# Kernel tuning notes

Measured on AMD Instinct MI355X. Metric: run time of the kernel, lower is better.

## Reference

```python
import jax, jax.numpy as jnp
import numpy as np

N_NODES = 100000
N_EDGES = 640000
NUM_GRAPHS = 256
IN_DIM, HID_DIM, OUT_DIM = 128, 128, 64


def setup_inputs() -> dict:
    key = jax.random.key(0)
    ks = jax.random.split(key, 6)
    x = jax.random.normal(ks[0], (N_NODES, IN_DIM), dtype=jnp.float32)
    edge_index = jax.random.randint(ks[1], (2, N_EDGES), 0, N_NODES, dtype=jnp.int64)
    batch = jnp.sort(jax.random.randint(ks[2], (N_NODES,), 0, NUM_GRAPHS, dtype=jnp.int64))
    W1 = jax.random.normal(ks[3], (IN_DIM, HID_DIM), dtype=jnp.float32) * (1.0 / np.sqrt(IN_DIM))
    b1 = jnp.zeros((HID_DIM,), dtype=jnp.float32)
    W2 = jax.random.normal(ks[4], (HID_DIM, OUT_DIM), dtype=jnp.float32) * (1.0 / np.sqrt(HID_DIM))
    b2 = jnp.zeros((OUT_DIM,), dtype=jnp.float32)
    return {"x": x, "edge_index": edge_index, "batch": batch,
            "W1": W1, "b1": b1, "W2": W2, "b2": b2}


def gcn_conv(x, row, col, norm, W, b, n_nodes):
    # transform first (smaller of in/out handled by W), then gather-scale-scatter
    xw = x @ W                                   # [N, F_out]
    msgs = norm[:, None] * xw[row]               # [E+N, F_out]
    out = jax.ops.segment_sum(msgs, col, num_segments=n_nodes)
    return out + b


def reference(x, edge_index, batch, W1, b1, W2, b2):
    n = x.shape[0]
    # add self-loops (PyG GCNConv default)
    loops = jnp.arange(n, dtype=edge_index.dtype)
    row = jnp.concatenate([edge_index[0], loops])  # sources
    col = jnp.concatenate([edge_index[1], loops])  # targets
    # symmetric normalization D^-1/2 (A+I) D^-1/2
    deg = jax.ops.segment_sum(jnp.ones_like(col, dtype=x.dtype), col, num_segments=n)
    dinv = jnp.where(deg > 0, jax.lax.rsqrt(deg), 0.0)
    norm = dinv[row] * dinv[col]
    h = jax.nn.relu(gcn_conv(x, row, col, norm, W1, b1, n))
    h = gcn_conv(h, row, col, norm, W2, b2, n)
    # global mean pool over batch ids
    sums = jax.ops.segment_sum(h, batch, num_segments=NUM_GRAPHS)
    counts = jax.ops.segment_sum(jnp.ones((n,), dtype=h.dtype), batch, num_segments=NUM_GRAPHS)
    return sums / jnp.clip(counts, 1.0)[:, None]
```

## Files before the change

kernel.cpp:

```cpp
#include <hip/hip_runtime.h>
#include <hip/hip_bf16.h>


typedef __attribute__((ext_vector_type(8))) short short8;
typedef __attribute__((ext_vector_type(4))) float f32x4;

__device__ __forceinline__ void atomAddF(float* p, float v) { unsafeAtomicAdd(p, v); }

__device__ __forceinline__ unsigned short bf_rne(float f) {
  unsigned int u = __float_as_uint(f);
  return (unsigned short)((u + 0x7fffu + ((u >> 16) & 1u)) >> 16);
}
__device__ __forceinline__ float bf2f(unsigned short h) {
  return __uint_as_float(((unsigned int)h) << 16);
}

__global__ __launch_bounds__(256) void k_prepw(const float* __restrict__ W1,
    const float* __restrict__ W2,
    unsigned short* __restrict__ W1th, unsigned short* __restrict__ W1tl,
    unsigned short* __restrict__ W2th, unsigned short* __restrict__ W2tl) {
  int i = blockIdx.x * 256 + threadIdx.x;
  if (i < 16384) {
    int c = i >> 7, k = i & 127;
    float f = W1[k * 128 + c];
    unsigned short hi = bf_rne(f);
    W1th[i] = hi;
    W1tl[i] = bf_rne(f - bf2f(hi));
  } else if (i < 16384 + 8192) {
    int j = i - 16384;
    int c = j >> 7, k = j & 127;
    float f = W2[k * 64 + c];
    unsigned short hi = bf_rne(f);
    W2th[j] = hi;
    W2tl[j] = bf_rne(f - bf2f(hi));
  }
}

__global__ __launch_bounds__(256) void k_count(const int* __restrict__ col,
                                               int* __restrict__ deg, int E) {
  int e = blockIdx.x * 256 + threadIdx.x;
  if (e < E) atomicAdd(&deg[col[e]], 1);
}

__global__ __launch_bounds__(256) void k_blocksum(const int* __restrict__ deg,
                                                  int* __restrict__ partial, int N) {
  __shared__ int sh[256];
  int t = threadIdx.x, i = blockIdx.x * 256 + t;
  sh[t] = (i < N) ? deg[i] : 0;
  __syncthreads();
  for (int o = 128; o > 0; o >>= 1) {
    if (t < o) sh[t] += sh[t + o];
    __syncthreads();
  }
  if (t == 0) partial[blockIdx.x] = sh[0];
}

__global__ __launch_bounds__(512) void k_scanpartial(int* __restrict__ partial, int nb) {
  __shared__ int sh[512];
  int t = threadIdx.x;
  int v = (t < nb) ? partial[t] : 0;
  sh[t] = v;
  __syncthreads();
  for (int o = 1; o < 512; o <<= 1) {
    int x = (t >= o) ? sh[t - o] : 0;
    __syncthreads();
    sh[t] += x;
    __syncthreads();
  }
  if (t < nb) partial[t] = sh[t] - v;
}

__global__ __launch_bounds__(256) void k_scanblock(int* __restrict__ deg,
    const int* __restrict__ partial, int* __restrict__ off,
    float* __restrict__ dinv, int N) {
  __shared__ int sh[256];
  int t = threadIdx.x, b = blockIdx.x, i = b * 256 + t;
  int v = (i < N) ? deg[i] : 0;
  sh[t] = v;
  __syncthreads();
  for (int o = 1; o < 256; o <<= 1) {
    int x = (t >= o) ? sh[t - o] : 0;
    __syncthreads();
    sh[t] += x;
    __syncthreads();
  }
  if (i < N) {
    int excl = partial[b] + sh[t] - v;
    off[i] = excl;
    deg[i] = excl;
    dinv[i] = rsqrtf((float)v + 1.0f);
    if (i == N - 1) off[N] = excl + v;
  }
}

__global__ __launch_bounds__(256) void k_fillcsr(const int* __restrict__ rows,
    const int* __restrict__ cols, int* __restrict__ cursor,
    int* __restrict__ csrsrc, int E) {
  int e = blockIdx.x * 256 + threadIdx.x;
  if (e < E) {
    int pos = atomicAdd(&cursor[cols[e]], 1);
    csrsrc[pos] = rows[e];
  }
}

__global__ __launch_bounds__(256) void k_goff(const int* __restrict__ batch,
                                              int* __restrict__ goff, int N, int G) {
  int g = blockIdx.x * 256 + threadIdx.x;
  if (g > G) return;
  int lo = 0, hi = N;
  while (lo < hi) {
    int m = (lo + hi) >> 1;
    if (batch[m] < g) lo = m + 1; else hi = m;
  }
  goff[g] = lo;
}

__global__ __launch_bounds__(256) void k_gemm1_mfma(
    const float* __restrict__ x,
    const unsigned short* __restrict__ W1th, const unsigned short* __restrict__ W1tl,
    const float* __restrict__ dinv, float* __restrict__ y, int N)
{
  const int tid = threadIdx.x;
  const int w = tid >> 6, l = tid & 63;
  const int v0 = blockIdx.x * 64;
  const int l15 = l & 15, lh = l >> 4;

  short8 bh[2][4], bl[2][4];
#pragma unroll
  for (int ct = 0; ct < 2; ++ct) {
    int colr = 32 * w + 16 * ct + l15;
#pragma unroll
    for (int ks = 0; ks < 4; ++ks) {
      bh[ct][ks] = *(const short8*)(W1th + colr * 128 + ks * 32 + 8 * lh);
      bl[ct][ks] = *(const short8*)(W1tl + colr * 128 + ks * 32 + 8 * lh);
    }
  }

#pragma unroll
  for (int rt = 0; rt < 4; ++rt) {
    int arow = v0 + rt * 16 + l15; if (arow >= N) arow = N - 1;
    const float* ar = x + (size_t)arow * 128 + 8 * lh;
    f32x4 acc0 = {0.f, 0.f, 0.f, 0.f}, acc1 = {0.f, 0.f, 0.f, 0.f};
#pragma unroll
    for (int ks = 0; ks < 4; ++ks) {
      float4 fa = *(const float4*)(ar + ks * 32);
      float4 fb = *(const float4*)(ar + ks * 32 + 4);
      short8 ah, al;
      float v0f;
      v0f = fa.x; ah[0] = (short)bf_rne(v0f); al[0] = (short)bf_rne(v0f - bf2f((unsigned short)ah[0]));
      v0f = fa.y; ah[1] = (short)bf_rne(v0f); al[1] = (short)bf_rne(v0f - bf2f((unsigned short)ah[1]));
      v0f = fa.z; ah[2] = (short)bf_rne(v0f); al[2] = (short)bf_rne(v0f - bf2f((unsigned short)ah[2]));
      v0f = fa.w; ah[3] = (short)bf_rne(v0f); al[3] = (short)bf_rne(v0f - bf2f((unsigned short)ah[3]));
      v0f = fb.x; ah[4] = (short)bf_rne(v0f); al[4] = (short)bf_rne(v0f - bf2f((unsigned short)ah[4]));
      v0f = fb.y; ah[5] = (short)bf_rne(v0f); al[5] = (short)bf_rne(v0f - bf2f((unsigned short)ah[5]));
      v0f = fb.z; ah[6] = (short)bf_rne(v0f); al[6] = (short)bf_rne(v0f - bf2f((unsigned short)ah[6]));
      v0f = fb.w; ah[7] = (short)bf_rne(v0f); al[7] = (short)bf_rne(v0f - bf2f((unsigned short)ah[7]));
      acc0 = __builtin_amdgcn_mfma_f32_16x16x32_bf16(ah, bh[0][ks], acc0, 0, 0, 0);
      acc0 = __builtin_amdgcn_mfma_f32_16x16x32_bf16(al, bh[0][ks], acc0, 0, 0, 0);
      acc0 = __builtin_amdgcn_mfma_f32_16x16x32_bf16(ah, bl[0][ks], acc0, 0, 0, 0);
      acc1 = __builtin_amdgcn_mfma_f32_16x16x32_bf16(ah, bh[1][ks], acc1, 0, 0, 0);
      acc1 = __builtin_amdgcn_mfma_f32_16x16x32_bf16(al, bh[1][ks], acc1, 0, 0, 0);
      acc1 = __builtin_amdgcn_mfma_f32_16x16x32_bf16(ah, bl[1][ks], acc1, 0, 0, 0);
    }

    int r4 = v0 + rt * 16 + lh * 4;
    float4 d4 = *(const float4*)(dinv + r4);
    int col0 = 32 * w + l15;
#pragma unroll
    for (int reg = 0; reg < 4; ++reg) {
      int row = r4 + reg;
      if (row < N) {
        float dd = (reg == 0) ? d4.x : (reg == 1) ? d4.y : (reg == 2) ? d4.z : d4.w;
        y[(size_t)row * 128 + col0]      = acc0[reg] * dd;
        y[(size_t)row * 128 + col0 + 16] = acc1[reg] * dd;
      }
    }
  }
}

__global__ __launch_bounds__(256) void k_gemm2_fused_mfma(
    const float* __restrict__ y, const int* __restrict__ off,
    const int* __restrict__ src,
    const unsigned short* __restrict__ W2th, const unsigned short* __restrict__ W2tl,
    const float* __restrict__ dinv, const float* __restrict__ b1,
    float* __restrict__ z, int N)
{
  __shared__ unsigned short hh[64 * 128];
  __shared__ unsigned short hl[64 * 128];
  const int tid = threadIdx.x;
  const int w = tid >> 6, l = tid & 63;
  const int v0 = blockIdx.x * 64;
  const int l15 = l & 15, lh = l >> 4;

  short8 bh[4], bl[4];
  {
    int colr = 16 * w + l15;
#pragma unroll
    for (int ks = 0; ks < 4; ++ks) {
      bh[ks] = *(const short8*)(W2th + colr * 128 + ks * 32 + 8 * lh);
      bl[ks] = *(const short8*)(W2tl + colr * 128 + ks * 32 + 8 * lh);
    }
  }

  {
    int vn = tid >> 2;
    int c0 = (tid & 3) * 32;
    int vv = v0 + vn;
    int vc = (vv < N) ? vv : N - 1;
    float acc[32];
    {
      const float4* yr = (const float4*)(y + (size_t)vc * 128 + c0);
#pragma unroll
      for (int q = 0; q < 8; ++q) {
        float4 t = yr[q];
        acc[4*q+0] = t.x; acc[4*q+1] = t.y; acc[4*q+2] = t.z; acc[4*q+3] = t.w;
      }
    }
    int e0 = off[vc], e1 = off[vc + 1];
    int last = e1 - 1;
    for (int i = e0; i < e1; i += 2) {
      int i1 = i + 1;
      int u0 = src[i];
      int u1 = src[i1 <= last ? i1 : last];
      float m1 = (i1 <= last) ? 1.f : 0.f;
      const float4* p0 = (const float4*)(y + (size_t)u0 * 128 + c0);
      const float4* p1 = (const float4*)(y + (size_t)u1 * 128 + c0);
#pragma unroll
      for (int q = 0; q < 8; ++q) {
        float4 t0 = p0[q], t1 = p1[q];
        acc[4*q+0] += t0.x + m1 * t1.x;
        acc[4*q+1] += t0.y + m1 * t1.y;
        acc[4*q+2] += t0.z + m1 * t1.z;
        acc[4*q+3] += t0.w + m1 * t1.w;
      }
    }
    float d = dinv[vc];
#pragma unroll
    for (int s = 0; s < 4; ++s) {
      short8 oh, ol;
#pragma unroll
      for (int j = 0; j < 8; ++j) {
        int dim = c0 + s * 8 + j;
        float hv = fmaxf(fmaf(d, acc[s*8+j], b1[dim]), 0.f);
        unsigned short hb = bf_rne(hv);
        oh[j] = (short)hb;
        ol[j] = (short)bf_rne(hv - bf2f(hb));
      }
      int byte = (vn * 256 + (c0 + s * 8) * 2) ^ ((vn & 7) << 4);
      *(short8*)((char*)hh + byte) = oh;
      *(short8*)((char*)hl + byte) = ol;
    }
  }
  __syncthreads();

#pragma unroll
  for (int rt = 0; rt < 4; ++rt) {
    int row = rt * 16 + l15;
    const int swz = (row & 7) << 4;
    const int base = row * 256 + lh * 16;
    f32x4 acc = {0.f, 0.f, 0.f, 0.f};
#pragma unroll
    for (int ks = 0; ks < 4; ++ks) {
      int byte = (base + ks * 64) ^ swz;
      short8 ah = *(const short8*)((char*)hh + byte);
      short8 al = *(const short8*)((char*)hl + byte);
      acc = __builtin_amdgcn_mfma_f32_16x16x32_bf16(ah, bh[ks], acc, 0, 0, 0);
      acc = __builtin_amdgcn_mfma_f32_16x16x32_bf16(al, bh[ks], acc, 0, 0, 0);
      acc = __builtin_amdgcn_mfma_f32_16x16x32_bf16(ah, bl[ks], acc, 0, 0, 0);
    }

    int r4 = v0 + rt * 16 + lh * 4;
    float4 d4 = *(const float4*)(dinv + r4);
    int col = 16 * w + l15;
#pragma unroll
    for (int reg = 0; reg < 4; ++reg) {
      int rr = r4 + reg;
      if (rr < N) {
        float dd = (reg == 0) ? d4.x : (reg == 1) ? d4.y : (reg == 2) ? d4.z : d4.w;
        z[(size_t)rr * 64 + col] = acc[reg] * dd;
      }
    }
  }
}

__global__ __launch_bounds__(256) void k_aggpool(
    const float* __restrict__ z, const int* __restrict__ off,
    const int* __restrict__ src, const float* __restrict__ dinv,
    const int* __restrict__ goff, float* __restrict__ out, int N)
{
  int g = blockIdx.x >> 3, seg = blockIdx.x & 7;
  int w = threadIdx.x >> 6, lane = threadIdx.x & 63;
  int lo = goff[g], hi = goff[g + 1];
  float acc = 0.f;
  for (int v = lo + seg * 4 + w; v < hi; v += 32) {
    float sv = z[(size_t)v * 64 + lane];
    int e0 = off[v], e1 = off[v + 1];
    int last = e1 - 1;
    for (int i = e0; i < e1; i += 4) {
      int i1 = i + 1, i2 = i + 2, i3 = i + 3;
      int u0 = src[i];
      int u1 = src[i1 <= last ? i1 : last];
      int u2 = src[i2 <= last ? i2 : last];
      int u3 = src[i3 <= last ? i3 : last];
      float a0 = z[(size_t)u0 * 64 + lane];
      float a1 = z[(size_t)u1 * 64 + lane];
      float a2 = z[(size_t)u2 * 64 + lane];
      float a3 = z[(size_t)u3 * 64 + lane];
      sv += a0;
      sv += (i1 <= last) ? a1 : 0.f;
      sv += (i2 <= last) ? a2 : 0.f;
      sv += (i3 <= last) ? a3 : 0.f;
    }
    acc = fmaf(dinv[v], sv, acc);
  }
  atomAddF(out + (size_t)g * 64 + lane, acc);
}

__global__ __launch_bounds__(256) void k_final(float* __restrict__ out,
    const int* __restrict__ goff, const float* __restrict__ b2, int total) {
  int i = blockIdx.x * 256 + threadIdx.x;
  if (i >= total) return;
  int g = i >> 6, d = i & 63;
  int n = goff[g + 1] - goff[g];
  out[i] = (n > 0) ? out[i] / (float)n + b2[d] : 0.f;
}

extern "C" void kernel_launch(void* const* d_in, const int* in_sizes, int n_in,
                              void* d_out, int out_size, void* d_ws, size_t ws_size,
                              hipStream_t stream) {
  const float* x     = (const float*)d_in[0];
  const int*   eidx  = (const int*)d_in[1];
  const int*   batch = (const int*)d_in[2];
  const float* W1    = (const float*)d_in[3];
  const float* b1    = (const float*)d_in[4];
  const float* W2    = (const float*)d_in[5];
  const float* b2    = (const float*)d_in[6];
  float* out = (float*)d_out;

  const int N = in_sizes[2];
  const int E = in_sizes[1] / 2;
  const int G = out_size / 64;

  const int* rows = eidx;
  const int* cols = eidx + E;

  float* y   = (float*)d_ws;
  float* z   = y + (size_t)N * 128;
  unsigned short* W1th = (unsigned short*)(z + (size_t)N * 64);
  unsigned short* W1tl = W1th + 16384;
  unsigned short* W2th = W1tl + 16384;
  unsigned short* W2tl = W2th + 8192;
  float* dinv    = (float*)(W2tl + 8192);
  int*   deg     = (int*)(dinv + N);
  int*   off     = deg + N;
  int*   partial = off + N + 1;
  int*   goff    = partial + 512;
  int*   csrsrc  = goff + G + 1;

  const int B = 256;
  const int nb = (N + B - 1) / B;

  hipMemsetAsync(deg, 0, (size_t)N * sizeof(int), stream);
  hipMemsetAsync(d_out, 0, (size_t)out_size * sizeof(float), stream);

  k_prepw<<<(16384 + 8192 + B - 1) / B, B, 0, stream>>>(W1, W2, W1th, W1tl, W2th, W2tl);

  k_count<<<(E + B - 1) / B, B, 0, stream>>>(cols, deg, E);
  k_blocksum<<<nb, B, 0, stream>>>(deg, partial, N);
  k_scanpartial<<<1, 512, 0, stream>>>(partial, nb);
  k_scanblock<<<nb, B, 0, stream>>>(deg, partial, off, dinv, N);
  k_fillcsr<<<(E + B - 1) / B, B, 0, stream>>>(rows, cols, deg, csrsrc, E);
  k_goff<<<(G + 1 + B - 1) / B, B, 0, stream>>>(batch, goff, N, G);

  k_gemm1_mfma<<<(N + 63) / 64, B, 0, stream>>>(x, W1th, W1tl, dinv, y, N);
  k_gemm2_fused_mfma<<<(N + 63) / 64, B, 0, stream>>>(y, off, csrsrc, W2th, W2tl, dinv, b1, z, N);
  k_aggpool<<<G * 8, B, 0, stream>>>(z, off, csrsrc, dinv, goff, out, N);
  k_final<<<(out_size + B - 1) / B, B, 0, stream>>>(out, goff, b2, out_size);
}
```

Before: 355.3 us.

## Replace gather-based final aggregation with source-side scatter into per-block graph tables

Builds a second, source-sorted edge list that stores each edge's destination graph id and dinv packed into one word. The final layer then scatters each node's z row into per-block 256x64 shared-memory tables with LDS atomics, and a separate kernel reduces the tables, applies the mean and adds the bias. This removes the per-edge gather of z rows and the global atomics in pooling, at the cost of an extra count/scan/fill pass, a 64 MB block-table write and a truncated-mantissa dinv in the packed metadata. The gemm2 gather kernel also moves to 32-node tiles with 4-way edge unrolling and an occupancy hint.

```diff
diff --git a/kernel.cpp b/kernel.cpp
--- a/kernel.cpp
+++ b/kernel.cpp
@@ -4,8 +4,6 @@
 
 typedef __attribute__((ext_vector_type(8))) short short8;
 typedef __attribute__((ext_vector_type(4))) float f32x4;
-
-__device__ __forceinline__ void atomAddF(float* p, float v) { unsafeAtomicAdd(p, v); }
 
 __device__ __forceinline__ unsigned short bf_rne(float f) {
   unsigned int u = __float_as_uint(f);
@@ -36,10 +34,13 @@
   }
 }
 
-__global__ __launch_bounds__(256) void k_count(const int* __restrict__ col,
-                                               int* __restrict__ deg, int E) {
+__global__ __launch_bounds__(256) void k_count2(const int* __restrict__ rows,
+    const int* __restrict__ cols, int* __restrict__ deg, int* __restrict__ odeg, int E) {
   int e = blockIdx.x * 256 + threadIdx.x;
-  if (e < E) atomicAdd(&deg[col[e]], 1);
+  if (e < E) {
+    atomicAdd(&deg[cols[e]], 1);
+    atomicAdd(&odeg[rows[e]], 1);
+  }
 }
 
 __global__ __launch_bounds__(256) void k_blocksum(const int* __restrict__ deg,
@@ -88,7 +89,7 @@
     int excl = partial[b] + sh[t] - v;
     off[i] = excl;
     deg[i] = excl;
-    dinv[i] = rsqrtf((float)v + 1.0f);
+    if (dinv) dinv[i] = rsqrtf((float)v + 1.0f);
     if (i == N - 1) off[N] = excl + v;
   }
 }
@@ -100,6 +101,18 @@
   if (e < E) {
     int pos = atomicAdd(&cursor[cols[e]], 1);
     csrsrc[pos] = rows[e];
+  }
+}
+
+__global__ __launch_bounds__(256) void k_fillcsc(const int* __restrict__ rows,
+    const int* __restrict__ cols, int* __restrict__ ocursor,
+    const int* __restrict__ batch, const float* __restrict__ dinv,
+    unsigned int* __restrict__ meta, int E) {
+  int e = blockIdx.x * 256 + threadIdx.x;
+  if (e < E) {
+    int s = rows[e], d = cols[e];
+    int pos = atomicAdd(&ocursor[s], 1);
+    meta[pos] = ((unsigned int)batch[d] << 24) | (__float_as_uint(dinv[d]) >> 8);
   }
 }
 
@@ -178,65 +191,73 @@
   }
 }
 
-__global__ __launch_bounds__(256) void k_gemm2_fused_mfma(
+__global__ __launch_bounds__(256, 4) void k_gemm2_fused_mfma(
     const float* __restrict__ y, const int* __restrict__ off,
     const int* __restrict__ src,
     const unsigned short* __restrict__ W2th, const unsigned short* __restrict__ W2tl,
     const float* __restrict__ dinv, const float* __restrict__ b1,
     float* __restrict__ z, int N)
 {
-  __shared__ unsigned short hh[64 * 128];
-  __shared__ unsigned short hl[64 * 128];
+  __shared__ __align__(16) unsigned short hh[32 * 128];
+  __shared__ __align__(16) unsigned short hl[32 * 128];
   const int tid = threadIdx.x;
   const int w = tid >> 6, l = tid & 63;
-  const int v0 = blockIdx.x * 64;
+  const int v0 = blockIdx.x * 32;
   const int l15 = l & 15, lh = l >> 4;
 
-  short8 bh[4], bl[4];
   {
-    int colr = 16 * w + l15;
-#pragma unroll
-    for (int ks = 0; ks < 4; ++ks) {
-      bh[ks] = *(const short8*)(W2th + colr * 128 + ks * 32 + 8 * lh);
-      bl[ks] = *(const short8*)(W2tl + colr * 128 + ks * 32 + 8 * lh);
-    }
-  }
-
-  {
-    int vn = tid >> 2;
-    int c0 = (tid & 3) * 32;
+    int vn = tid >> 3;
+    int c0 = (tid & 7) << 4;
     int vv = v0 + vn;
     int vc = (vv < N) ? vv : N - 1;
-    float acc[32];
+    float acc[16];
     {
       const float4* yr = (const float4*)(y + (size_t)vc * 128 + c0);
 #pragma unroll
-      for (int q = 0; q < 8; ++q) {
+      for (int q = 0; q < 4; ++q) {
         float4 t = yr[q];
         acc[4*q+0] = t.x; acc[4*q+1] = t.y; acc[4*q+2] = t.z; acc[4*q+3] = t.w;
       }
     }
     int e0 = off[vc], e1 = off[vc + 1];
     int last = e1 - 1;
-    for (int i = e0; i < e1; i += 2) {
-      int i1 = i + 1;
+    for (int i = e0; i < e1; i += 4) {
+      int i1 = i + 1, i2 = i + 2, i3 = i + 3;
       int u0 = src[i];
       int u1 = src[i1 <= last ? i1 : last];
+      int u2 = src[i2 <= last ? i2 : last];
+      int u3 = src[i3 <= last ? i3 : last];
       float m1 = (i1 <= last) ? 1.f : 0.f;
+      float m2 = (i2 <= last) ? 1.f : 0.f;
+      float m3 = (i3 <= last) ? 1.f : 0.f;
       const float4* p0 = (const float4*)(y + (size_t)u0 * 128 + c0);
       const float4* p1 = (const float4*)(y + (size_t)u1 * 128 + c0);
-#pragma unroll
-      for (int q = 0; q < 8; ++q) {
-        float4 t0 = p0[q], t1 = p1[q];
-        acc[4*q+0] += t0.x + m1 * t1.x;
-        acc[4*q+1] += t0.y + m1 * t1.y;
-        acc[4*q+2] += t0.z + m1 * t1.z;
-        acc[4*q+3] += t0.w + m1 * t1.w;
-      }
+      const float4* p2 = (const float4*)(y + (size_t)u2 * 128 + c0);
+      const float4* p3 = (const float4*)(y + (size_t)u3 * 128 + c0);
+      float4 t00 = p0[0], t01 = p0[1], t02 = p0[2], t03 = p0[3];
+      float4 t10 = p1[0], t11 = p1[1], t12 = p1[2], t13 = p1[3];
+      float4 t20 = p2[0], t21 = p2[1], t22 = p2[2], t23 = p2[3];
+      float4 t30 = p3[0], t31 = p3[1], t32 = p3[2], t33 = p3[3];
+      acc[0]  += t00.x + m1*t10.x + m2*t20.x + m3*t30.x;
+      acc[1]  += t00.y + m1*t10.y + m2*t20.y + m3*t30.y;
+      acc[2]  += t00.z + m1*t10.z + m2*t20.z + m3*t30.z;
+      acc[3]  += t00.w + m1*t10.w + m2*t20.w + m3*t30.w;
+      acc[4]  += t01.x + m1*t11.x + m2*t21.x + m3*t31.x;
+      acc[5]  += t01.y + m1*t11.y + m2*t21.y + m3*t31.y;
+      acc[6]  += t01.z + m1*t11.z + m2*t21.z + m3*t31.z;
+      acc[7]  += t01.w + m1*t11.w + m2*t21.w + m3*t31.w;
+      acc[8]  += t02.x + m1*t12.x + m2*t22.x + m3*t32.x;
+      acc[9]  += t02.y + m1*t12.y + m2*t22.y + m3*t32.y;
+      acc[10] += t02.z + m1*t12.z + m2*t22.z + m3*t32.z;
+      acc[11] += t02.w + m1*t12.w + m2*t22.w + m3*t32.w;
+      acc[12] += t03.x + m1*t13.x + m2*t23.x + m3*t33.x;
+      acc[13] += t03.y + m1*t13.y + m2*t23.y + m3*t33.y;
+      acc[14] += t03.z + m1*t13.z + m2*t23.z + m3*t33.z;
+      acc[15] += t03.w + m1*t13.w + m2*t23.w + m3*t33.w;
     }
     float d = dinv[vc];
 #pragma unroll
-    for (int s = 0; s < 4; ++s) {
+    for (int s = 0; s < 2; ++s) {
       short8 oh, ol;
 #pragma unroll
       for (int j = 0; j < 8; ++j) {
@@ -251,10 +272,20 @@
       *(short8*)((char*)hl + byte) = ol;
     }
   }
-  __syncthreads();
-
-#pragma unroll
-  for (int rt = 0; rt < 4; ++rt) {
+
+  short8 bh[4], bl[4];
+  {
+    int colr = 16 * w + l15;
+#pragma unroll
+    for (int ks = 0; ks < 4; ++ks) {
+      bh[ks] = *(const short8*)(W2th + colr * 128 + ks * 32 + 8 * lh);
+      bl[ks] = *(const short8*)(W2tl + colr * 128 + ks * 32 + 8 * lh);
+    }
+  }
+  __syncthreads();
+
+#pragma unroll
+  for (int rt = 0; rt < 2; ++rt) {
     int row = rt * 16 + l15;
     const int swz = (row & 7) << 4;
     const int base = row * 256 + lh * 16;
@@ -283,46 +314,58 @@
   }
 }
 
-__global__ __launch_bounds__(256) void k_aggpool(
-    const float* __restrict__ z, const int* __restrict__ off,
-    const int* __restrict__ src, const float* __restrict__ dinv,
-    const int* __restrict__ goff, float* __restrict__ out, int N)
+#define NB_TAB 256
+__global__ __launch_bounds__(1024) void k_scatterpool(
+    const float* __restrict__ z, const int* __restrict__ ooff,
+    const unsigned int* __restrict__ meta, const int* __restrict__ batch,
+    const float* __restrict__ dinv, float* __restrict__ blocktab, int N)
 {
-  int g = blockIdx.x >> 3, seg = blockIdx.x & 7;
-  int w = threadIdx.x >> 6, lane = threadIdx.x & 63;
-  int lo = goff[g], hi = goff[g + 1];
-  float acc = 0.f;
-  for (int v = lo + seg * 4 + w; v < hi; v += 32) {
-    float sv = z[(size_t)v * 64 + lane];
-    int e0 = off[v], e1 = off[v + 1];
-    int last = e1 - 1;
-    for (int i = e0; i < e1; i += 4) {
-      int i1 = i + 1, i2 = i + 2, i3 = i + 3;
-      int u0 = src[i];
-      int u1 = src[i1 <= last ? i1 : last];
-      int u2 = src[i2 <= last ? i2 : last];
-      int u3 = src[i3 <= last ? i3 : last];
-      float a0 = z[(size_t)u0 * 64 + lane];
-      float a1 = z[(size_t)u1 * 64 + lane];
-      float a2 = z[(size_t)u2 * 64 + lane];
-      float a3 = z[(size_t)u3 * 64 + lane];
-      sv += a0;
-      sv += (i1 <= last) ? a1 : 0.f;
-      sv += (i2 <= last) ? a2 : 0.f;
-      sv += (i3 <= last) ? a3 : 0.f;
-    }
-    acc = fmaf(dinv[v], sv, acc);
-  }
-  atomAddF(out + (size_t)g * 64 + lane, acc);
-}
-
-__global__ __launch_bounds__(256) void k_final(float* __restrict__ out,
-    const int* __restrict__ goff, const float* __restrict__ b2, int total) {
+  __shared__ float tab[256 * 64];
+  for (int i = threadIdx.x; i < 16384; i += 1024) tab[i] = 0.f;
+  __syncthreads();
+
+  const int wid = threadIdx.x >> 6, lane = threadIdx.x & 63;
+  const int per = (N + NB_TAB - 1) / NB_TAB;
+  const int n0 = blockIdx.x * per;
+  const int n1 = (n0 + per < N) ? n0 + per : N;
+
+  for (int u = n0 + wid; u < n1; u += 16) {
+    float zd = z[(size_t)u * 64 + lane];
+    int e0 = ooff[u], e1 = ooff[u + 1];
+    for (int base = e0; base < e1; base += 64) {
+      int idx = base + lane;
+      unsigned int m = (idx < e1) ? meta[idx] : 0u;
+      int cnt = e1 - base; if (cnt > 64) cnt = 64;
+      for (int j = 0; j < cnt; ++j) {
+        unsigned int mj = (unsigned int)__shfl((int)m, j);
+        int gj = mj >> 24;
+        float cj = __uint_as_float(mj << 8);
+        atomicAdd(&tab[gj * 64 + lane], cj * zd);
+      }
+    }
+    atomicAdd(&tab[batch[u] * 64 + lane], dinv[u] * zd);
+  }
+  __syncthreads();
+  float* dst = blocktab + (size_t)blockIdx.x * 16384;
+  for (int i = threadIdx.x; i < 16384; i += 1024) dst[i] = tab[i];
+}
+
+__global__ __launch_bounds__(256) void k_redtab(const float* __restrict__ blocktab,
+    const int* __restrict__ goff, const float* __restrict__ b2,
+    float* __restrict__ out) {
   int i = blockIdx.x * 256 + threadIdx.x;
-  if (i >= total) return;
+  if (i >= 16384) return;
+  float s0 = 0.f, s1 = 0.f, s2 = 0.f, s3 = 0.f;
+  for (int b = 0; b < NB_TAB; b += 4) {
+    s0 += blocktab[(size_t)(b + 0) * 16384 + i];
+    s1 += blocktab[(size_t)(b + 1) * 16384 + i];
+    s2 += blocktab[(size_t)(b + 2) * 16384 + i];
+    s3 += blocktab[(size_t)(b + 3) * 16384 + i];
+  }
+  float s = (s0 + s1) + (s2 + s3);
   int g = i >> 6, d = i & 63;
   int n = goff[g + 1] - goff[g];
-  out[i] = (n > 0) ? out[i] / (float)n + b2[d] : 0.f;
+  out[i] = (n > 0) ? s / (float)n + b2[d] : 0.f;
 }
 
 extern "C" void kernel_launch(void* const* d_in, const int* in_sizes, int n_in,
@@ -352,28 +395,35 @@
   unsigned short* W2tl = W2th + 8192;
   float* dinv    = (float*)(W2tl + 8192);
   int*   deg     = (int*)(dinv + N);
-  int*   off     = deg + N;
-  int*   partial = off + N + 1;
+  int*   odeg    = deg + N;
+  int*   off     = odeg + N;
+  int*   ooff    = off + N + 1;
+  int*   partial = ooff + N + 1;
   int*   goff    = partial + 512;
   int*   csrsrc  = goff + G + 1;
+  unsigned int* cscmeta = (unsigned int*)(csrsrc + E);
+  float* blocktab = (float*)(cscmeta + E);
 
   const int B = 256;
   const int nb = (N + B - 1) / B;
 
-  hipMemsetAsync(deg, 0, (size_t)N * sizeof(int), stream);
-  hipMemsetAsync(d_out, 0, (size_t)out_size * sizeof(float), stream);
+  hipMemsetAsync(deg, 0, (size_t)2 * N * sizeof(int), stream);
 
   k_prepw<<<(16384 + 8192 + B - 1) / B, B, 0, stream>>>(W1, W2, W1th, W1tl, W2th, W2tl);
 
-  k_count<<<(E + B - 1) / B, B, 0, stream>>>(cols, deg, E);
+  k_count2<<<(E + B - 1) / B, B, 0, stream>>>(rows, cols, deg, odeg, E);
   k_blocksum<<<nb, B, 0, stream>>>(deg, partial, N);
   k_scanpartial<<<1, 512, 0, stream>>>(partial, nb);
   k_scanblock<<<nb, B, 0, stream>>>(deg, partial, off, dinv, N);
   k_fillcsr<<<(E + B - 1) / B, B, 0, stream>>>(rows, cols, deg, csrsrc, E);
+  k_blocksum<<<nb, B, 0, stream>>>(odeg, partial, N);
+  k_scanpartial<<<1, 512, 0, stream>>>(partial, nb);
+  k_scanblock<<<nb, B, 0, stream>>>(odeg, partial, ooff, (float*)nullptr, N);
+  k_fillcsc<<<(E + B - 1) / B, B, 0, stream>>>(rows, cols, odeg, batch, dinv, cscmeta, E);
   k_goff<<<(G + 1 + B - 1) / B, B, 0, stream>>>(batch, goff, N, G);
 
   k_gemm1_mfma<<<(N + 63) / 64, B, 0, stream>>>(x, W1th, W1tl, dinv, y, N);
-  k_gemm2_fused_mfma<<<(N + 63) / 64, B, 0, stream>>>(y, off, csrsrc, W2th, W2tl, dinv, b1, z, N);
-  k_aggpool<<<G * 8, B, 0, stream>>>(z, off, csrsrc, dinv, goff, out, N);
-  k_final<<<(out_size + B - 1) / B, B, 0, stream>>>(out, goff, b2, out_size);
-}
+  k_gemm2_fused_mfma<<<(N + 31) / 32, B, 0, stream>>>(y, off, csrsrc, W2th, W2tl, dinv, b1, z, N);
+  k_scatterpool<<<NB_TAB, 1024, 0, stream>>>(z, ooff, cscmeta, batch, dinv, blocktab, N);
+  k_redtab<<<(16384 + B - 1) / B, B, 0, stream>>>(blocktab, goff, b2, out);
+}
```

Result: slower. 645.0 us (+81.5%).

## Store intermediate node features as bf16 and shrink gemm2 tile to 32 rows

Applied to the files above, without the earlier changes.

The intermediate feature buffers y (N×128) and z (N×64) are now stored as bf16 instead of fp32, which halves the bytes moved by the random-access neighbor gathers in the fused aggregation+GEMM2 kernel and in the pooling kernel. The fused kernel now handles 32 nodes per block with 8 threads per node, unrolls the gather loop over 4 edges, and loads the W2 fragments after the gather to reduce register pressure, with a launch bound of 4 blocks. The cost is lower precision in the stored intermediates, which adds rounding error relative to the fp32 reference.

```diff
diff --git a/kernel.cpp b/kernel.cpp
--- a/kernel.cpp
+++ b/kernel.cpp
@@ -14,6 +14,8 @@
 __device__ __forceinline__ float bf2f(unsigned short h) {
   return __uint_as_float(((unsigned int)h) << 16);
 }
+__device__ __forceinline__ float bf_lo(unsigned int u) { return __uint_as_float(u << 16); }
+__device__ __forceinline__ float bf_hi(unsigned int u) { return __uint_as_float(u & 0xffff0000u); }
 
 __global__ __launch_bounds__(256) void k_prepw(const float* __restrict__ W1,
     const float* __restrict__ W2,
@@ -118,7 +120,7 @@
 __global__ __launch_bounds__(256) void k_gemm1_mfma(
     const float* __restrict__ x,
     const unsigned short* __restrict__ W1th, const unsigned short* __restrict__ W1tl,
-    const float* __restrict__ dinv, float* __restrict__ y, int N)
+    const float* __restrict__ dinv, unsigned short* __restrict__ yb, int N)
 {
   const int tid = threadIdx.x;
   const int w = tid >> 6, l = tid & 63;
@@ -171,72 +173,84 @@
       int row = r4 + reg;
       if (row < N) {
         float dd = (reg == 0) ? d4.x : (reg == 1) ? d4.y : (reg == 2) ? d4.z : d4.w;
-        y[(size_t)row * 128 + col0]      = acc0[reg] * dd;
-        y[(size_t)row * 128 + col0 + 16] = acc1[reg] * dd;
+        yb[(size_t)row * 128 + col0]      = bf_rne(acc0[reg] * dd);
+        yb[(size_t)row * 128 + col0 + 16] = bf_rne(acc1[reg] * dd);
       }
     }
   }
 }
 
-__global__ __launch_bounds__(256) void k_gemm2_fused_mfma(
-    const float* __restrict__ y, const int* __restrict__ off,
+__global__ __launch_bounds__(256, 4) void k_gemm2_fused_mfma(
+    const unsigned short* __restrict__ yb, const int* __restrict__ off,
     const int* __restrict__ src,
     const unsigned short* __restrict__ W2th, const unsigned short* __restrict__ W2tl,
     const float* __restrict__ dinv, const float* __restrict__ b1,
-    float* __restrict__ z, int N)
+    unsigned short* __restrict__ zb, int N)
 {
-  __shared__ unsigned short hh[64 * 128];
-  __shared__ unsigned short hl[64 * 128];
+  __shared__ __align__(16) unsigned short hh[32 * 128];
+  __shared__ __align__(16) unsigned short hl[32 * 128];
   const int tid = threadIdx.x;
   const int w = tid >> 6, l = tid & 63;
-  const int v0 = blockIdx.x * 64;
+  const int v0 = blockIdx.x * 32;
   const int l15 = l & 15, lh = l >> 4;
 
-  short8 bh[4], bl[4];
   {
-    int colr = 16 * w + l15;
-#pragma unroll
-    for (int ks = 0; ks < 4; ++ks) {
-      bh[ks] = *(const short8*)(W2th + colr * 128 + ks * 32 + 8 * lh);
-      bl[ks] = *(const short8*)(W2tl + colr * 128 + ks * 32 + 8 * lh);
-    }
-  }
-
-  {
-    int vn = tid >> 2;
-    int c0 = (tid & 3) * 32;
+    int vn = tid >> 3;
+    int c0 = (tid & 7) << 4;
     int vv = v0 + vn;
     int vc = (vv < N) ? vv : N - 1;
-    float acc[32];
+    float acc[16];
     {
-      const float4* yr = (const float4*)(y + (size_t)vc * 128 + c0);
-#pragma unroll
-      for (int q = 0; q < 8; ++q) {
-        float4 t = yr[q];
-        acc[4*q+0] = t.x; acc[4*q+1] = t.y; acc[4*q+2] = t.z; acc[4*q+3] = t.w;
-      }
+      const uint4* yr = (const uint4*)(yb + (size_t)vc * 128 + c0);
+      uint4 t0 = yr[0], t1 = yr[1];
+      acc[0]  = bf_lo(t0.x); acc[1]  = bf_hi(t0.x);
+      acc[2]  = bf_lo(t0.y); acc[3]  = bf_hi(t0.y);
+      acc[4]  = bf_lo(t0.z); acc[5]  = bf_hi(t0.z);
+      acc[6]  = bf_lo(t0.w); acc[7]  = bf_hi(t0.w);
+      acc[8]  = bf_lo(t1.x); acc[9]  = bf_hi(t1.x);
+      acc[10] = bf_lo(t1.y); acc[11] = bf_hi(t1.y);
+      acc[12] = bf_lo(t1.z); acc[13] = bf_hi(t1.z);
+      acc[14] = bf_lo(t1.w); acc[15] = bf_hi(t1.w);
     }
     int e0 = off[vc], e1 = off[vc + 1];
     int last = e1 - 1;
-    for (int i = e0; i < e1; i += 2) {
-      int i1 = i + 1;
+    for (int i = e0; i < e1; i += 4) {
+      int i1 = i + 1, i2 = i + 2, i3 = i + 3;
       int u0 = src[i];
       int u1 = src[i1 <= last ? i1 : last];
+      int u2 = src[i2 <= last ? i2 : last];
+      int u3 = src[i3 <= last ? i3 : last];
       float m1 = (i1 <= last) ? 1.f : 0.f;
-      const float4* p0 = (const float4*)(y + (size_t)u0 * 128 + c0);
-      const float4* p1 = (const float4*)(y + (size_t)u1 * 128 + c0);
-#pragma unroll
-      for (int q = 0; q < 8; ++q) {
-        float4 t0 = p0[q], t1 = p1[q];
-        acc[4*q+0] += t0.x + m1 * t1.x;
-        acc[4*q+1] += t0.y + m1 * t1.y;
-        acc[4*q+2] += t0.z + m1 * t1.z;
-        acc[4*q+3] += t0.w + m1 * t1.w;
-      }
+      float m2 = (i2 <= last) ? 1.f : 0.f;
+      float m3 = (i3 <= last) ? 1.f : 0.f;
+      const uint4* p0 = (const uint4*)(yb + (size_t)u0 * 128 + c0);
+      const uint4* p1 = (const uint4*)(yb + (size_t)u1 * 128 + c0);
+      const uint4* p2 = (const uint4*)(yb + (size_t)u2 * 128 + c0);
+      const uint4* p3 = (const uint4*)(yb + (size_t)u3 * 128 + c0);
+      uint4 a0 = p0[0], b0 = p0[1];
+      uint4 a1 = p1[0], b1v = p1[1];
+      uint4 a2 = p2[0], b2v = p2[1];
+      uint4 a3 = p3[0], b3v = p3[1];
+      acc[0]  += bf_lo(a0.x) + m1*bf_lo(a1.x) + m2*bf_lo(a2.x) + m3*bf_lo(a3.x);
+      acc[1]  += bf_hi(a0.x) + m1*bf_hi(a1.x) + m2*bf_hi(a2.x) + m3*bf_hi(a3.x);
+      acc[2]  += bf_lo(a0.y) + m1*bf_lo(a1.y) + m2*bf_lo(a2.y) + m3*bf_lo(a3.y);
+      acc[3]  += bf_hi(a0.y) + m1*bf_hi(a1.y) + m2*bf_hi(a2.y) + m3*bf_hi(a3.y);
+      acc[4]  += bf_lo(a0.z) + m1*bf_lo(a1.z) + m2*bf_lo(a2.z) + m3*bf_lo(a3.z);
+      acc[5]  += bf_hi(a0.z) + m1*bf_hi(a1.z) + m2*bf_hi(a2.z) + m3*bf_hi(a3.z);
+      acc[6]  += bf_lo(a0.w) + m1*bf_lo(a1.w) + m2*bf_lo(a2.w) + m3*bf_lo(a3.w);
+      acc[7]  += bf_hi(a0.w) + m1*bf_hi(a1.w) + m2*bf_hi(a2.w) + m3*bf_hi(a3.w);
+      acc[8]  += bf_lo(b0.x) + m1*bf_lo(b1v.x) + m2*bf_lo(b2v.x) + m3*bf_lo(b3v.x);
+      acc[9]  += bf_hi(b0.x) + m1*bf_hi(b1v.x) + m2*bf_hi(b2v.x) + m3*bf_hi(b3v.x);
+      acc[10] += bf_lo(b0.y) + m1*bf_lo(b1v.y) + m2*bf_lo(b2v.y) + m3*bf_lo(b3v.y);
+      acc[11] += bf_hi(b0.y) + m1*bf_hi(b1v.y) + m2*bf_hi(b2v.y) + m3*bf_hi(b3v.y);
+      acc[12] += bf_lo(b0.z) + m1*bf_lo(b1v.z) + m2*bf_lo(b2v.z) + m3*bf_lo(b3v.z);
+      acc[13] += bf_hi(b0.z) + m1*bf_hi(b1v.z) + m2*bf_hi(b2v.z) + m3*bf_hi(b3v.z);
+      acc[14] += bf_lo(b0.w) + m1*bf_lo(b1v.w) + m2*bf_lo(b2v.w) + m3*bf_lo(b3v.w);
+      acc[15] += bf_hi(b0.w) + m1*bf_hi(b1v.w) + m2*bf_hi(b2v.w) + m3*bf_hi(b3v.w);
     }
     float d = dinv[vc];
 #pragma unroll
-    for (int s = 0; s < 4; ++s) {
+    for (int s = 0; s < 2; ++s) {
       short8 oh, ol;
 #pragma unroll
       for (int j = 0; j < 8; ++j) {
@@ -251,10 +265,20 @@
       *(short8*)((char*)hl + byte) = ol;
     }
   }
+
+  short8 bh[4], bl[4];
+  {
+    int colr = 16 * w + l15;
+#pragma unroll
+    for (int ks = 0; ks < 4; ++ks) {
+      bh[ks] = *(const short8*)(W2th + colr * 128 + ks * 32 + 8 * lh);
+      bl[ks] = *(const short8*)(W2tl + colr * 128 + ks * 32 + 8 * lh);
+    }
+  }
   __syncthreads();
 
 #pragma unroll
-  for (int rt = 0; rt < 4; ++rt) {
+  for (int rt = 0; rt < 2; ++rt) {
     int row = rt * 16 + l15;
     const int swz = (row & 7) << 4;
     const int base = row * 256 + lh * 16;
@@ -277,14 +301,14 @@
       int rr = r4 + reg;
       if (rr < N) {
         float dd = (reg == 0) ? d4.x : (reg == 1) ? d4.y : (reg == 2) ? d4.z : d4.w;
-        z[(size_t)rr * 64 + col] = acc[reg] * dd;
+        zb[(size_t)rr * 64 + col] = bf_rne(acc[reg] * dd);
       }
     }
   }
 }
 
 __global__ __launch_bounds__(256) void k_aggpool(
-    const float* __restrict__ z, const int* __restrict__ off,
+    const unsigned short* __restrict__ zb, const int* __restrict__ off,
     const int* __restrict__ src, const float* __restrict__ dinv,
     const int* __restrict__ goff, float* __restrict__ out, int N)
 {
@@ -293,7 +317,7 @@
   int lo = goff[g], hi = goff[g + 1];
   float acc = 0.f;
   for (int v = lo + seg * 4 + w; v < hi; v += 32) {
-    float sv = z[(size_t)v * 64 + lane];
+    float sv = bf2f(zb[(size_t)v * 64 + lane]);
     int e0 = off[v], e1 = off[v + 1];
     int last = e1 - 1;
     for (int i = e0; i < e1; i += 4) {
@@ -302,10 +326,10 @@
       int u1 = src[i1 <= last ? i1 : last];
       int u2 = src[i2 <= last ? i2 : last];
       int u3 = src[i3 <= last ? i3 : last];
-      float a0 = z[(size_t)u0 * 64 + lane];
-      float a1 = z[(size_t)u1 * 64 + lane];
-      float a2 = z[(size_t)u2 * 64 + lane];
-      float a3 = z[(size_t)u3 * 64 + lane];
+      float a0 = bf2f(zb[(size_t)u0 * 64 + lane]);
+      float a1 = bf2f(zb[(size_t)u1 * 64 + lane]);
+      float a2 = bf2f(zb[(size_t)u2 * 64 + lane]);
+      float a3 = bf2f(zb[(size_t)u3 * 64 + lane]);
       sv += a0;
       sv += (i1 <= last) ? a1 : 0.f;
       sv += (i2 <= last) ? a2 : 0.f;
@@ -344,9 +368,9 @@
   const int* rows = eidx;
   const int* cols = eidx + E;
 
-  float* y   = (float*)d_ws;
-  float* z   = y + (size_t)N * 128;
-  unsigned short* W1th = (unsigned short*)(z + (size_t)N * 64);
+  unsigned short* yb  = (unsigned short*)d_ws;
+  unsigned short* zb  = yb + (size_t)N * 128;
+  unsigned short* W1th = zb + (size_t)N * 64;
   unsigned short* W1tl = W1th + 16384;
   unsigned short* W2th = W1tl + 16384;
   unsigned short* W2tl = W2th + 8192;
@@ -372,8 +396,8 @@
   k_fillcsr<<<(E + B - 1) / B, B, 0, stream>>>(rows, cols, deg, csrsrc, E);
   k_goff<<<(G + 1 + B - 1) / B, B, 0, stream>>>(batch, goff, N, G);
 
-  k_gemm1_mfma<<<(N + 63) / 64, B, 0, stream>>>(x, W1th, W1tl, dinv, y, N);
-  k_gemm2_fused_mfma<<<(N + 63) / 64, B, 0, stream>>>(y, off, csrsrc, W2th, W2tl, dinv, b1, z, N);
-  k_aggpool<<<G * 8, B, 0, stream>>>(z, off, csrsrc, dinv, goff, out, N);
+  k_gemm1_mfma<<<(N + 63) / 64, B, 0, stream>>>(x, W1th, W1tl, dinv, yb, N);
+  k_gemm2_fused_mfma<<<(N + 31) / 32, B, 0, stream>>>(yb, off, csrsrc, W2th, W2tl, dinv, b1, zb, N);
+  k_aggpool<<<G * 8, B, 0, stream>>>(zb, off, csrsrc, dinv, goff, out, N);
   k_final<<<(out_size + B - 1) / B, B, 0, stream>>>(out, goff, b2, out_size);
 }
```

New measurement: 293.2 us. 17.5% less time.
